# Kernel optimization log

Hardware: AMD Instinct MI355X
Metric: run time of the kernel (lower is better)

Reference implementation:

```python
import jax, jax.numpy as jnp
import numpy as np

DIM = 1024
HEADS = 16
DIM_HEAD = 64
INNER = HEADS * DIM_HEAD  # 1024
EPS = 1e-5


def setup_inputs() -> dict:
    key = jax.random.key(0)
    ks = jax.random.split(key, 5)
    x = jax.random.normal(ks[0], (4, 2048, DIM), dtype=jnp.float32)
    ln_gamma = jnp.ones((DIM,), dtype=jnp.float32)
    ln_beta = jnp.zeros((DIM,), dtype=jnp.float32)
    # nn.Linear weights ~ U(-1/sqrt(fan_in), 1/sqrt(fan_in)); stored as (out, in) in torch,
    # here kept as (in, out) for x @ W.
    lim = 1.0 / np.sqrt(DIM)
    w_qkv = jax.random.uniform(ks[1], (DIM, 3 * INNER), minval=-lim, maxval=lim, dtype=jnp.float32)
    lim2 = 1.0 / np.sqrt(INNER)
    w_out = jax.random.uniform(ks[2], (INNER, DIM), minval=-lim2, maxval=lim2, dtype=jnp.float32)
    return {"x": x, "ln_gamma": ln_gamma, "ln_beta": ln_beta, "w_qkv": w_qkv, "w_out": w_out}


def reference(x, ln_gamma, ln_beta, w_qkv, w_out):
    b, n, d = x.shape
    # LayerNorm
    mu = jnp.mean(x, axis=-1, keepdims=True)
    var = jnp.mean(jnp.square(x - mu), axis=-1, keepdims=True)
    xn = (x - mu) * jax.lax.rsqrt(var + EPS) * ln_gamma + ln_beta
    # QKV projection
    qkv = xn @ w_qkv  # (b, n, 3*inner)
    q, k, v = jnp.split(qkv, 3, axis=-1)
    def to_heads(t):
        return t.reshape(b, n, HEADS, DIM_HEAD).transpose(0, 2, 1, 3)  # (b,h,n,dh)
    q, k, v = to_heads(q), to_heads(k), to_heads(v)
    scale = DIM_HEAD ** -0.5
    scores = jnp.einsum('bhqd,bhkd->bhqk', q, k) * scale
    causal = jnp.tril(jnp.ones((n, n), dtype=bool))
    scores = jnp.where(causal, scores, -jnp.inf)
    probs = jax.nn.softmax(scores, axis=-1)
    out = jnp.einsum('bhqk,bhkd->bhqd', probs, v)
    out = out.transpose(0, 2, 1, 3).reshape(b, n, INNER)
    return out @ w_out
```

## Files before the change

kernel.cpp:

```cpp
#include <hip/hip_runtime.h>
#include <hip/hip_bf16.h>

#define DIM 1024
#define HEADS 16
#define DH 64
#define SEQ 2048
#define BATCH 4
#define ROWS (BATCH * SEQ)
#define NQKV (3 * DIM)

typedef __attribute__((ext_vector_type(8))) __bf16 bf16x8;
typedef __attribute__((ext_vector_type(4))) __bf16 bf16x4;
typedef __attribute__((ext_vector_type(4))) float f32x4;

__device__ inline void gload16(const void* g, void* l) {
  __builtin_amdgcn_global_load_lds(
      (const __attribute__((address_space(1))) void*)g,
      (__attribute__((address_space(3))) void*)l, 16, 0, 0);
}

__global__ __launch_bounds__(256) void ln_kernel(
    const float* __restrict__ x, const float* __restrict__ gamma,
    const float* __restrict__ beta, __bf16* __restrict__ xnb) {
  const int row = blockIdx.x;
  const int tid = threadIdx.x;
  const float4* xr = (const float4*)(x + (size_t)row * DIM);
  float4 v = xr[tid];
  float s1 = v.x + v.y + v.z + v.w;
  float s2 = v.x * v.x + v.y * v.y + v.z * v.z + v.w * v.w;
#pragma unroll
  for (int d = 32; d > 0; d >>= 1) {
    s1 += __shfl_xor(s1, d);
    s2 += __shfl_xor(s2, d);
  }
  __shared__ float red1[4], red2[4];
  const int wave = tid >> 6, lane = tid & 63;
  if (lane == 0) { red1[wave] = s1; red2[wave] = s2; }
  __syncthreads();
  s1 = red1[0] + red1[1] + red1[2] + red1[3];
  s2 = red2[0] + red2[1] + red2[2] + red2[3];
  const float mean = s1 * (1.0f / DIM);
  const float var = s2 * (1.0f / DIM) - mean * mean;
  const float rstd = rsqrtf(var + 1e-5f);
  float4 g = ((const float4*)gamma)[tid];
  float4 b = ((const float4*)beta)[tid];
  bf16x4 o;
  o[0] = (__bf16)((v.x - mean) * rstd * g.x + b.x);
  o[1] = (__bf16)((v.y - mean) * rstd * g.y + b.y);
  o[2] = (__bf16)((v.z - mean) * rstd * g.z + b.z);
  o[3] = (__bf16)((v.w - mean) * rstd * g.w + b.w);
  *(bf16x4*)(xnb + (size_t)row * DIM + tid * 4) = o;
}

__global__ __launch_bounds__(256) void transpose_cast(
    const float* __restrict__ in, __bf16* __restrict__ outT, int rows, int cols) {
  __shared__ float tile[32][33];
  const int tx = threadIdx.x & 31, ty = threadIdx.x >> 5;
  const int c0 = blockIdx.x * 32, r0 = blockIdx.y * 32;
#pragma unroll
  for (int rr = ty; rr < 32; rr += 8)
    tile[rr][tx] = in[(size_t)(r0 + rr) * cols + c0 + tx];
  __syncthreads();
#pragma unroll
  for (int rr = ty; rr < 32; rr += 8)
    outT[(size_t)(c0 + rr) * rows + r0 + tx] = (__bf16)tile[tx][rr];
}

template <int MODE>
__global__ __launch_bounds__(256) void gemm128(
    const __bf16* __restrict__ A, const __bf16* __restrict__ Bt, int K, int N,
    float* __restrict__ Cout, __bf16* __restrict__ qb, __bf16* __restrict__ kb,
    __bf16* __restrict__ vtb) {
  __shared__ __bf16 smem[64 * 136];
  __bf16* As = smem;
  __bf16* Bs = smem + 4096;
  const int tid = threadIdx.x;
  const int wave = tid >> 6, lane = tid & 63;
  const int quad = lane >> 4, l16 = lane & 15;
  const int wm = wave >> 1, wn = wave & 1;
  const size_t tileM = (size_t)blockIdx.x * 128;
  const size_t tileN = (size_t)blockIdx.y * 128;

  f32x4 acc[4][4];
#pragma unroll
  for (int i = 0; i < 4; ++i)
#pragma unroll
    for (int j = 0; j < 4; ++j) acc[i][j] = (f32x4){0.f, 0.f, 0.f, 0.f};

  const int sr = lane >> 2;
  const int sc = lane & 3;
  const int ck = (l16 >> 1) & 3;

  for (int k0 = 0; k0 < K; k0 += 32) {
    __syncthreads();
#pragma unroll
    for (int p = 0; p < 2; ++p) {
      const int rbase = p * 64 + wave * 16;
      const int row = rbase + sr;
      const int gc = (sc ^ ((row >> 1) & 3)) << 3;
      gload16(A + (tileM + row) * (size_t)K + k0 + gc, &As[rbase * 32]);
      gload16(Bt + (tileN + row) * (size_t)K + k0 + gc, &Bs[rbase * 32]);
    }
    __syncthreads();
    bf16x8 af[4], bfr[4];
#pragma unroll
    for (int mt = 0; mt < 4; ++mt)
      af[mt] = *(const bf16x8*)&As[(wm * 64 + mt * 16 + l16) * 32 + ((quad ^ ck) << 3)];
#pragma unroll
    for (int nt = 0; nt < 4; ++nt)
      bfr[nt] = *(const bf16x8*)&Bs[(wn * 64 + nt * 16 + l16) * 32 + ((quad ^ ck) << 3)];
#pragma unroll
    for (int mt = 0; mt < 4; ++mt)
#pragma unroll
      for (int nt = 0; nt < 4; ++nt)
        acc[mt][nt] = __builtin_amdgcn_mfma_f32_16x16x32_bf16(af[mt], bfr[nt],
                                                              acc[mt][nt], 0, 0, 0);
  }

  if (MODE == 0) {
#pragma unroll
    for (int mt = 0; mt < 4; ++mt)
#pragma unroll
      for (int nt = 0; nt < 4; ++nt) {
        const size_t c = tileN + wn * 64 + nt * 16 + l16;
#pragma unroll
        for (int r = 0; r < 4; ++r) {
          const size_t m = tileM + wm * 64 + mt * 16 + quad * 4 + r;
          Cout[m * (size_t)N + c] = acc[mt][nt][r];
        }
      }
  } else {
    const int sel = (int)(tileN >> 10);
    if (sel < 2) {
      __bf16* dst = (sel == 0) ? qb : kb;
#pragma unroll
      for (int mt = 0; mt < 4; ++mt)
#pragma unroll
        for (int nt = 0; nt < 4; ++nt) {
          const int c = (int)(tileN & 1023) + wn * 64 + nt * 16 + l16;
          const int head = c >> 6, dh = c & 63;
#pragma unroll
          for (int r = 0; r < 4; ++r) {
            const size_t m = tileM + wm * 64 + mt * 16 + quad * 4 + r;
            const int b = (int)(m >> 11), seq = (int)(m & 2047);
            dst[(((size_t)b * HEADS + head) * SEQ + seq) * DH + dh] =
                (__bf16)acc[mt][nt][r];
          }
        }
    } else {
      const int b = (int)(tileM >> 11);
      const int seq0 = (int)(tileM & 2047);
      const int headbase = (int)((tileN & 1023) >> 6);
#pragma unroll
      for (int h = 0; h < 2; ++h) {
        __syncthreads();
        if (wn == h) {
#pragma unroll
          for (int mt = 0; mt < 4; ++mt)
#pragma unroll
            for (int nt = 0; nt < 4; ++nt)
#pragma unroll
              for (int r = 0; r < 4; ++r)
                smem[(nt * 16 + l16) * 136 + wm * 64 + mt * 16 + quad * 4 + r] =
                    (__bf16)acc[mt][nt][r];
        }
        __syncthreads();
        const int rr = tid >> 2;
        const int m0 = (tid & 3) * 32;
        __bf16* dst = vtb + (((size_t)b * HEADS + headbase + h) * DH + rr) * SEQ +
                      seq0 + m0;
#pragma unroll
        for (int q = 0; q < 4; ++q)
          *(bf16x8*)(dst + q * 8) = *(const bf16x8*)&smem[rr * 136 + m0 + q * 8];
      }
    }
  }
}

__global__ __launch_bounds__(256) void attn_kernel(
    const __bf16* __restrict__ qb, const __bf16* __restrict__ kb,
    const __bf16* __restrict__ vtb, __bf16* __restrict__ ob) {
  const int bx = blockIdx.x;
  const int bh = blockIdx.y;
  const int tid = threadIdx.x;
  const int wave = tid >> 6, lane = tid & 63;
  const int quad = lane >> 4, l16 = lane & 15;

  __shared__ __bf16 Ks[2][128 * 64];
  __shared__ __bf16 Vs[2][64 * 128];
  __shared__ __bf16 Ps[4][32 * 36];

  const __bf16* kg = kb + (size_t)bh * SEQ * DH;
  const __bf16* vg = vtb + (size_t)bh * DH * SEQ;

  const int i1 = bx, i2 = 15 - bx;
  const int T = 17;

  const int kr = lane >> 3, kc = lane & 7;
  const int vr = lane >> 4, vc = lane & 15;

  auto stage = [&](int buf, int j) {
#pragma unroll
    for (int p = 0; p < 4; ++p) {
      const int rbase = p * 32 + wave * 8;
      const int row = rbase + kr;
      gload16(kg + (size_t)(j * 128 + row) * DH + ((kc ^ (row & 7)) << 3),
              &Ks[buf][rbase * 64]);
    }
#pragma unroll
    for (int p = 0; p < 4; ++p) {
      const int rbase = p * 16 + wave * 4;
      const int row = rbase + vr;
      gload16(vg + (size_t)row * SEQ + j * 128 + ((vc ^ (row & 7)) << 3),
              &Vs[buf][rbase * 128]);
    }
  };

  const float QSCALE = 0.125f * 1.44269504088896f;
  bf16x8 qf[2][2];
  auto load_q = [&](int i) {
    const __bf16* qbase = qb + ((size_t)bh * SEQ + (size_t)i * 128 + wave * 32) * DH;
#pragma unroll
    for (int mt = 0; mt < 2; ++mt)
#pragma unroll
      for (int ks = 0; ks < 2; ++ks) {
        bf16x8 v = *(const bf16x8*)(qbase + (mt * 16 + l16) * DH + ks * 32 + quad * 8);
#pragma unroll
        for (int e = 0; e < 8; ++e) v[e] = (__bf16)((float)v[e] * QSCALE);
        qf[mt][ks] = v;
      }
  };

  float m_i[2], l_i[2];
  f32x4 o_acc[4][2];
  auto reset_state = [&]() {
#pragma unroll
    for (int mt = 0; mt < 2; ++mt) { m_i[mt] = -1e30f; l_i[mt] = 0.f; }
#pragma unroll
    for (int md = 0; md < 4; ++md)
#pragma unroll
      for (int mt = 0; mt < 2; ++mt) o_acc[md][mt] = (f32x4){0.f, 0.f, 0.f, 0.f};
  };
  const int b_out = bh >> 4, h_out = bh & 15;
  auto epilogue = [&](int i) {
#pragma unroll
    for (int mt = 0; mt < 2; ++mt) {
      const float inv = __builtin_amdgcn_rcpf(l_i[mt]);
      const int seq = i * 128 + wave * 32 + mt * 16 + l16;
      __bf16* dst = ob + ((size_t)b_out * SEQ + seq) * DIM + h_out * DH;
#pragma unroll
      for (int md = 0; md < 4; ++md) {
        bf16x4 pk;
#pragma unroll
        for (int r = 0; r < 4; ++r) pk[r] = (__bf16)(o_acc[md][mt][r] * inv);
        *(bf16x4*)(dst + md * 16 + quad * 4) = pk;
      }
    }
  };

  load_q(i1);
  reset_state();
  stage(0, 0);

  for (int t = 0; t < T; ++t) {
    __syncthreads();
    if (t + 1 < T) {
      const int jn = (t + 1 <= bx) ? (t + 1) : (t - bx);
      stage((t + 1) & 1, jn);
    }
    const int buf = t & 1;
    const int i = (t <= bx) ? i1 : i2;
    const int j = (t <= bx) ? t : (t - bx - 1);
    const bool diag = (j == i);

    f32x4 sa[8][2];
#pragma unroll
    for (int nt = 0; nt < 8; ++nt)
#pragma unroll
      for (int mt = 0; mt < 2; ++mt) sa[nt][mt] = (f32x4){0.f, 0.f, 0.f, 0.f};
#pragma unroll
    for (int nt = 0; nt < 8; ++nt)
#pragma unroll
      for (int ks = 0; ks < 2; ++ks) {
        bf16x8 kf = *(const bf16x8*)&Ks[buf][(nt * 16 + l16) * 64 +
                                            (((ks * 4 + quad) ^ (l16 & 7)) << 3)];
#pragma unroll
        for (int mt = 0; mt < 2; ++mt)
          sa[nt][mt] =
              __builtin_amdgcn_mfma_f32_16x16x32_bf16(kf, qf[mt][ks], sa[nt][mt], 0, 0, 0);
      }

    if (diag) {
#pragma unroll
      for (int nt = 0; nt < 8; ++nt)
#pragma unroll
        for (int mt = 0; mt < 2; ++mt) {
          const int qrow = wave * 32 + mt * 16 + l16;
#pragma unroll
          for (int r = 0; r < 4; ++r) {
            const int kv = nt * 16 + quad * 4 + r;
            if (kv > qrow) sa[nt][mt][r] = -1e30f;
          }
        }
    }

    float alpha[2];
#pragma unroll
    for (int mt = 0; mt < 2; ++mt) {
      float mx = -1e30f;
#pragma unroll
      for (int nt = 0; nt < 8; ++nt)
#pragma unroll
        for (int r = 0; r < 4; ++r) mx = fmaxf(mx, sa[nt][mt][r]);
      mx = fmaxf(mx, __shfl_xor(mx, 16));
      mx = fmaxf(mx, __shfl_xor(mx, 32));
      const float mnew = fmaxf(m_i[mt], mx);
      alpha[mt] = exp2f(m_i[mt] - mnew);
      m_i[mt] = mnew;
      float rs = 0.f;
#pragma unroll
      for (int nt = 0; nt < 8; ++nt)
#pragma unroll
        for (int r = 0; r < 4; ++r) {
          const float p = exp2f(sa[nt][mt][r] - mnew);
          sa[nt][mt][r] = p;
          rs += p;
        }
      rs += __shfl_xor(rs, 16);
      rs += __shfl_xor(rs, 32);
      l_i[mt] = l_i[mt] * alpha[mt] + rs;
    }
#pragma unroll
    for (int md = 0; md < 4; ++md)
#pragma unroll
      for (int mt = 0; mt < 2; ++mt)
#pragma unroll
        for (int r = 0; r < 4; ++r) o_acc[md][mt][r] *= alpha[mt];

#pragma unroll
    for (int c = 0; c < 4; ++c) {
#pragma unroll
      for (int mt = 0; mt < 2; ++mt)
#pragma unroll
        for (int ntl = 0; ntl < 2; ++ntl) {
          const int nt = c * 2 + ntl;
          bf16x4 pk;
#pragma unroll
          for (int r = 0; r < 4; ++r) pk[r] = (__bf16)sa[nt][mt][r];
          *(bf16x4*)&Ps[wave][(mt * 16 + l16) * 36 + ntl * 16 + quad * 4] = pk;
        }
      bf16x8 pf[2];
#pragma unroll
      for (int mt = 0; mt < 2; ++mt)
        pf[mt] = *(const bf16x8*)&Ps[wave][(mt * 16 + l16) * 36 + quad * 8];
#pragma unroll
      for (int md = 0; md < 4; ++md) {
        bf16x8 vf = *(const bf16x8*)&Vs[buf][(md * 16 + l16) * 128 +
                                            (((c * 4 + quad) ^ (l16 & 7)) << 3)];
#pragma unroll
        for (int mt = 0; mt < 2; ++mt)
          o_acc[md][mt] =
              __builtin_amdgcn_mfma_f32_16x16x32_bf16(vf, pf[mt], o_acc[md][mt], 0, 0, 0);
      }
    }

    if (t == bx) {
      epilogue(i1);
      reset_state();
      load_q(i2);
    }
  }
  epilogue(i2);
}

extern "C" void kernel_launch(void* const* d_in, const int* in_sizes, int n_in,
                              void* d_out, int out_size, void* d_ws, size_t ws_size,
                              hipStream_t stream) {
  const float* x = (const float*)d_in[0];
  const float* gamma = (const float*)d_in[1];
  const float* beta = (const float*)d_in[2];
  const float* w_qkv = (const float*)d_in[3];
  const float* w_out = (const float*)d_in[4];
  float* out = (float*)d_out;

  char* ws = (char*)d_ws;
  const size_t MB = 1024 * 1024;
  __bf16* xnb = (__bf16*)ws;
  __bf16* wqkvT = (__bf16*)(ws + 16 * MB);
  __bf16* woutT = (__bf16*)(ws + 24 * MB);
  __bf16* qbuf = (__bf16*)(ws + 32 * MB);
  __bf16* kbuf = (__bf16*)(ws + 48 * MB);
  __bf16* vtbuf = (__bf16*)(ws + 64 * MB);
  __bf16* attnb = xnb;

  ln_kernel<<<ROWS, 256, 0, stream>>>(x, gamma, beta, xnb);
  transpose_cast<<<dim3(NQKV / 32, DIM / 32), 256, 0, stream>>>(w_qkv, wqkvT, DIM, NQKV);
  transpose_cast<<<dim3(DIM / 32, DIM / 32), 256, 0, stream>>>(w_out, woutT, DIM, DIM);
  gemm128<1><<<dim3(ROWS / 128, NQKV / 128), 256, 0, stream>>>(
      xnb, wqkvT, DIM, NQKV, nullptr, qbuf, kbuf, vtbuf);
  attn_kernel<<<dim3(8, BATCH * HEADS), 256, 0, stream>>>(qbuf, kbuf, vtbuf, attnb);
  gemm128<0><<<dim3(ROWS / 128, DIM / 128), 256, 0, stream>>>(
      attnb, woutT, DIM, DIM, out, nullptr, nullptr, nullptr);
}
```

Before: 320.6 us.

## Vectorize GEMM epilogues via swapped MFMA operands, defer row-sum reduction, reorder attention grid

The GEMM swaps the MFMA A/B operands for non-V tiles, so each lane holds four consecutive columns. This lets the Q/K and output epilogues use vector stores instead of scalar ones. The V-transpose epilogue now writes bf16x4 directly and no longer stages through shared memory with extra barriers. The attention kernel delays the cross-lane row-sum reduction to the epilogue, uses the hardware exp2 builtin, and swaps grid dimensions so blocks of the same query tile across heads are scheduled together. Risks include less-coalesced V-transpose stores and small precision differences from the raw exp2 instruction.

After: 321.4 us. About the same (+0.2%).

```diff
diff --git a/kernel.cpp b/kernel.cpp
--- a/kernel.cpp
+++ b/kernel.cpp
@@ -17,6 +17,14 @@
   __builtin_amdgcn_global_load_lds(
       (const __attribute__((address_space(1))) void*)g,
       (__attribute__((address_space(3))) void*)l, 16, 0, 0);
+}
+
+__device__ inline float fast_exp2(float x) {
+#if __has_builtin(__builtin_amdgcn_exp2f)
+  return __builtin_amdgcn_exp2f(x);
+#else
+  return exp2f(x);
+#endif
 }
 
 __global__ __launch_bounds__(256) void ln_kernel(
@@ -71,15 +79,16 @@
     const __bf16* __restrict__ A, const __bf16* __restrict__ Bt, int K, int N,
     float* __restrict__ Cout, __bf16* __restrict__ qb, __bf16* __restrict__ kb,
     __bf16* __restrict__ vtb) {
-  __shared__ __bf16 smem[64 * 136];
-  __bf16* As = smem;
-  __bf16* Bs = smem + 4096;
+  __shared__ __bf16 As[128 * 32];
+  __shared__ __bf16 Bs[128 * 32];
   const int tid = threadIdx.x;
   const int wave = tid >> 6, lane = tid & 63;
   const int quad = lane >> 4, l16 = lane & 15;
   const int wm = wave >> 1, wn = wave & 1;
   const size_t tileM = (size_t)blockIdx.x * 128;
   const size_t tileN = (size_t)blockIdx.y * 128;
+  const int sel = (MODE == 1) ? (int)(tileN >> 10) : 0;
+  const bool vmode = (MODE == 1) && (sel == 2);
 
   f32x4 acc[4][4];
 #pragma unroll
@@ -109,69 +118,62 @@
 #pragma unroll
     for (int nt = 0; nt < 4; ++nt)
       bfr[nt] = *(const bf16x8*)&Bs[(wn * 64 + nt * 16 + l16) * 32 + ((quad ^ ck) << 3)];
-#pragma unroll
-    for (int mt = 0; mt < 4; ++mt)
-#pragma unroll
-      for (int nt = 0; nt < 4; ++nt)
-        acc[mt][nt] = __builtin_amdgcn_mfma_f32_16x16x32_bf16(af[mt], bfr[nt],
-                                                              acc[mt][nt], 0, 0, 0);
+    if (vmode) {
+#pragma unroll
+      for (int mt = 0; mt < 4; ++mt)
+#pragma unroll
+        for (int nt = 0; nt < 4; ++nt)
+          acc[mt][nt] = __builtin_amdgcn_mfma_f32_16x16x32_bf16(af[mt], bfr[nt],
+                                                                acc[mt][nt], 0, 0, 0);
+    } else {
+#pragma unroll
+      for (int mt = 0; mt < 4; ++mt)
+#pragma unroll
+        for (int nt = 0; nt < 4; ++nt)
+          acc[mt][nt] = __builtin_amdgcn_mfma_f32_16x16x32_bf16(bfr[nt], af[mt],
+                                                                acc[mt][nt], 0, 0, 0);
+    }
   }
 
   if (MODE == 0) {
 #pragma unroll
-    for (int mt = 0; mt < 4; ++mt)
+    for (int mt = 0; mt < 4; ++mt) {
+      const size_t m = tileM + wm * 64 + mt * 16 + l16;
 #pragma unroll
       for (int nt = 0; nt < 4; ++nt) {
-        const size_t c = tileN + wn * 64 + nt * 16 + l16;
-#pragma unroll
-        for (int r = 0; r < 4; ++r) {
-          const size_t m = tileM + wm * 64 + mt * 16 + quad * 4 + r;
-          Cout[m * (size_t)N + c] = acc[mt][nt][r];
-        }
-      }
+        const size_t n0 = tileN + wn * 64 + nt * 16 + quad * 4;
+        *(f32x4*)&Cout[m * (size_t)N + n0] = acc[mt][nt];
+      }
+    }
+  } else if (sel < 2) {
+    __bf16* dst = (sel == 0) ? qb : kb;
+#pragma unroll
+    for (int mt = 0; mt < 4; ++mt) {
+      const size_t m = tileM + wm * 64 + mt * 16 + l16;
+      const int b = (int)(m >> 11), seq = (int)(m & 2047);
+#pragma unroll
+      for (int nt = 0; nt < 4; ++nt) {
+        const int c = (int)(tileN & 1023) + wn * 64 + nt * 16 + quad * 4;
+        const int head = c >> 6, dh = c & 63;
+        bf16x4 pk;
+#pragma unroll
+        for (int r = 0; r < 4; ++r) pk[r] = (__bf16)acc[mt][nt][r];
+        *(bf16x4*)&dst[(((size_t)b * HEADS + head) * SEQ + seq) * DH + dh] = pk;
+      }
+    }
   } else {
-    const int sel = (int)(tileN >> 10);
-    if (sel < 2) {
-      __bf16* dst = (sel == 0) ? qb : kb;
-#pragma unroll
-      for (int mt = 0; mt < 4; ++mt)
-#pragma unroll
-        for (int nt = 0; nt < 4; ++nt) {
-          const int c = (int)(tileN & 1023) + wn * 64 + nt * 16 + l16;
-          const int head = c >> 6, dh = c & 63;
-#pragma unroll
-          for (int r = 0; r < 4; ++r) {
-            const size_t m = tileM + wm * 64 + mt * 16 + quad * 4 + r;
-            const int b = (int)(m >> 11), seq = (int)(m & 2047);
-            dst[(((size_t)b * HEADS + head) * SEQ + seq) * DH + dh] =
-                (__bf16)acc[mt][nt][r];
-          }
-        }
-    } else {
-      const int b = (int)(tileM >> 11);
-      const int seq0 = (int)(tileM & 2047);
-      const int headbase = (int)((tileN & 1023) >> 6);
-#pragma unroll
-      for (int h = 0; h < 2; ++h) {
-        __syncthreads();
-        if (wn == h) {
-#pragma unroll
-          for (int mt = 0; mt < 4; ++mt)
-#pragma unroll
-            for (int nt = 0; nt < 4; ++nt)
-#pragma unroll
-              for (int r = 0; r < 4; ++r)
-                smem[(nt * 16 + l16) * 136 + wm * 64 + mt * 16 + quad * 4 + r] =
-                    (__bf16)acc[mt][nt][r];
-        }
-        __syncthreads();
-        const int rr = tid >> 2;
-        const int m0 = (tid & 3) * 32;
-        __bf16* dst = vtb + (((size_t)b * HEADS + headbase + h) * DH + rr) * SEQ +
-                      seq0 + m0;
-#pragma unroll
-        for (int q = 0; q < 4; ++q)
-          *(bf16x8*)(dst + q * 8) = *(const bf16x8*)&smem[rr * 136 + m0 + q * 8];
+#pragma unroll
+    for (int nt = 0; nt < 4; ++nt) {
+      const int c = (int)(tileN & 1023) + wn * 64 + nt * 16 + l16;
+      const int head = c >> 6, dh = c & 63;
+#pragma unroll
+      for (int mt = 0; mt < 4; ++mt) {
+        const size_t m0 = tileM + wm * 64 + mt * 16 + quad * 4;
+        const int b = (int)(m0 >> 11), seq = (int)(m0 & 2047);
+        bf16x4 pk;
+#pragma unroll
+        for (int r = 0; r < 4; ++r) pk[r] = (__bf16)acc[mt][nt][r];
+        *(bf16x4*)&vtb[(((size_t)b * HEADS + head) * DH + dh) * SEQ + seq] = pk;
       }
     }
   }
@@ -180,8 +182,8 @@
 __global__ __launch_bounds__(256) void attn_kernel(
     const __bf16* __restrict__ qb, const __bf16* __restrict__ kb,
     const __bf16* __restrict__ vtb, __bf16* __restrict__ ob) {
-  const int bx = blockIdx.x;
-  const int bh = blockIdx.y;
+  const int bh = blockIdx.x;
+  const int bx = blockIdx.y;
   const int tid = threadIdx.x;
   const int wave = tid >> 6, lane = tid & 63;
   const int quad = lane >> 4, l16 = lane & 15;
@@ -245,7 +247,10 @@
   auto epilogue = [&](int i) {
 #pragma unroll
     for (int mt = 0; mt < 2; ++mt) {
-      const float inv = __builtin_amdgcn_rcpf(l_i[mt]);
+      float lsum = l_i[mt];
+      lsum += __shfl_xor(lsum, 16);
+      lsum += __shfl_xor(lsum, 32);
+      const float inv = __builtin_amdgcn_rcpf(lsum);
       const int seq = i * 128 + wave * 32 + mt * 16 + l16;
       __bf16* dst = ob + ((size_t)b_out * SEQ + seq) * DIM + h_out * DH;
 #pragma unroll
@@ -315,19 +320,17 @@
       mx = fmaxf(mx, __shfl_xor(mx, 16));
       mx = fmaxf(mx, __shfl_xor(mx, 32));
       const float mnew = fmaxf(m_i[mt], mx);
-      alpha[mt] = exp2f(m_i[mt] - mnew);
+      alpha[mt] = fast_exp2(m_i[mt] - mnew);
       m_i[mt] = mnew;
       float rs = 0.f;
 #pragma unroll
       for (int nt = 0; nt < 8; ++nt)
 #pragma unroll
         for (int r = 0; r < 4; ++r) {
-          const float p = exp2f(sa[nt][mt][r] - mnew);
+          const float p = fast_exp2(sa[nt][mt][r] - mnew);
           sa[nt][mt][r] = p;
           rs += p;
         }
-      rs += __shfl_xor(rs, 16);
-      rs += __shfl_xor(rs, 32);
       l_i[mt] = l_i[mt] * alpha[mt] + rs;
     }
 #pragma unroll
@@ -398,7 +401,7 @@
   transpose_cast<<<dim3(DIM / 32, DIM / 32), 256, 0, stream>>>(w_out, woutT, DIM, DIM);
   gemm128<1><<<dim3(ROWS / 128, NQKV / 128), 256, 0, stream>>>(
       xnb, wqkvT, DIM, NQKV, nullptr, qbuf, kbuf, vtbuf);
-  attn_kernel<<<dim3(8, BATCH * HEADS), 256, 0, stream>>>(qbuf, kbuf, vtbuf, attnb);
+  attn_kernel<<<dim3(BATCH * HEADS, 8), 256, 0, stream>>>(qbuf, kbuf, vtbuf, attnb);
   gemm128<0><<<dim3(ROWS / 128, DIM / 128), 256, 0, stream>>>(
       attnb, woutT, DIM, DIM, out, nullptr, nullptr, nullptr);
 }
```
